# Kernel optimization log

Measured on AMD Instinct MI355X. Metric: run time of the kernel, lower is better.

The kernel has to match this reference:

```python
import jax, jax.numpy as jnp
import numpy as np

N, E, B = 100000, 1600000, 1024
F, H, C = 9, 4, 32
CH, L = 30, 20

def _leaky(x, slope):
    return jnp.where(x >= 0, x, slope * x)

def _add_self_loops(edge_index, n):
    ar = jnp.arange(n, dtype=edge_index.dtype)
    return jnp.concatenate([edge_index, jnp.stack([ar, ar])], axis=1)

def _gat_conv(x, edge_index, W, att_src, att_dst, bias):
    # PyG GATConv, concat heads, eval mode (no attn dropout), self loops
    n = x.shape[0]
    ei = _add_self_loops(edge_index, n)
    src, dst = ei[0], ei[1]
    h = (x @ W).reshape(n, H, C)                      # [N,H,C]
    a_s = jnp.sum(h * att_src, axis=-1)               # [N,H]
    a_d = jnp.sum(h * att_dst, axis=-1)               # [N,H]
    e = _leaky(a_s[src] + a_d[dst], 0.2)              # [Etot,H]
    m = jax.ops.segment_max(e, dst, num_segments=n)
    ex = jnp.exp(e - m[dst])
    s = jax.ops.segment_sum(ex, dst, num_segments=n)
    alpha = ex / (s[dst] + 1e-16)                     # softmax per dst node/head
    msg = h[src] * alpha[:, :, None]                  # [Etot,H,C]
    out = jax.ops.segment_sum(msg, dst, num_segments=n)
    return out.reshape(n, H * C) + bias

def _gcn_conv(x, edge_index, W, bias):
    # PyG GCNConv: self loops + symmetric normalization
    n = x.shape[0]
    ei = _add_self_loops(edge_index, n)
    src, dst = ei[0], ei[1]
    deg = jax.ops.segment_sum(jnp.ones(ei.shape[1], x.dtype), dst, num_segments=n)
    dinv = jnp.where(deg > 0, jax.lax.rsqrt(deg), 0.0)
    norm = dinv[src] * dinv[dst]                      # [Etot]
    h = x @ W
    out = jax.ops.segment_sum(h[src] * norm[:, None], dst, num_segments=n)
    return out + bias

def _global_mean_pool(x, batch, b):
    s = jax.ops.segment_sum(x, batch, num_segments=b)
    cnt = jax.ops.segment_sum(jnp.ones(x.shape[0], x.dtype), batch, num_segments=b)
    return s / jnp.maximum(cnt, 1.0)[:, None]

def _conv1d(x, w, b):
    # x: [B,Cin,L], w: [Cout,Cin,K], VALID conv
    y = jax.lax.conv_general_dilated(x, w, (1,), 'VALID',
                                     dimension_numbers=('NCH', 'OIH', 'NCH'))
    return y + b[None, :, None]

def _bn_eval(x, g, be, m, v):
    return (x - m[None, :, None]) * jax.lax.rsqrt(v[None, :, None] + 1e-5) * g[None, :, None] + be[None, :, None]

def _forward(x, seq_data, W_gat, att_src, att_dst, b_gat, W2, b2, W3, b3,
             conv1_w, conv1_b, conv2_w, conv2_b,
             bn1_g, bn1_b, bn1_m, bn1_v, bn2_g, bn2_b, bn2_m, bn2_v,
             fc1_W, fc1_b, fus_W, fus_b, cls1_W, cls1_b, cls3_W, cls3_b,
             edge_index, batch):
    slope = 0.01  # nn.LeakyReLU default
    # graph branch
    g = _leaky(_gat_conv(x, edge_index, W_gat, att_src, att_dst, b_gat), slope)
    g = _leaky(_gcn_conv(g, edge_index, W2, b2), slope)
    g = _leaky(_gcn_conv(g, edge_index, W3, b3), slope)
    g = _global_mean_pool(g, batch, B)                # [B,128]
    # sequence branch (eval mode: dropout = identity, BN uses running stats)
    s = _conv1d(seq_data, conv1_w, conv1_b)           # [B,64,18]
    s = _leaky(_bn_eval(s, bn1_g, bn1_b, bn1_m, bn1_v), slope)
    s = _conv1d(s, conv2_w, conv2_b)                  # [B,64,16]
    s = _leaky(_bn_eval(s, bn2_g, bn2_b, bn2_m, bn2_v), slope)
    s = s.reshape(s.shape[0], -1) @ fc1_W + fc1_b     # [B,64]
    # fusion + classifier
    comb = jnp.concatenate([g, s], axis=1)            # [B,192]
    comb = _leaky(comb @ fus_W + fus_b, slope)
    comb = _leaky(comb @ cls1_W + cls1_b, slope)
    return comb @ cls3_W + cls3_b                     # [B,1]

def setup_inputs():
    key = jax.random.key(0)
    ks = jax.random.split(key, 20)
    rn = lambda k, s, sc=0.1: jax.random.normal(k, s, dtype=jnp.float32) * sc
    return {
        'x': rn(ks[0], (N, F), 1.0),
        'edge_index': jax.random.randint(ks[1], (2, E), 0, N, dtype=jnp.int32),
        'batch': jnp.sort(jax.random.randint(ks[2], (N,), 0, B, dtype=jnp.int32)),
        'seq_data': rn(ks[3], (B, CH, L), 1.0),
        'W_gat': rn(ks[4], (F, H * C)), 'att_src': rn(ks[5], (H, C)),
        'att_dst': rn(ks[6], (H, C)), 'b_gat': jnp.zeros(H * C, jnp.float32),
        'W2': rn(ks[7], (H * C, 64)), 'b2': jnp.zeros(64, jnp.float32),
        'W3': rn(ks[8], (64, 128)), 'b3': jnp.zeros(128, jnp.float32),
        'conv1_w': rn(ks[9], (64, CH, 3)), 'conv1_b': jnp.zeros(64, jnp.float32),
        'conv2_w': rn(ks[10], (64, 64, 3)), 'conv2_b': jnp.zeros(64, jnp.float32),
        'bn1_g': jnp.ones(64, jnp.float32), 'bn1_b': jnp.zeros(64, jnp.float32),
        'bn1_m': jnp.zeros(64, jnp.float32), 'bn1_v': jnp.ones(64, jnp.float32),
        'bn2_g': jnp.ones(64, jnp.float32), 'bn2_b': jnp.zeros(64, jnp.float32),
        'bn2_m': jnp.zeros(64, jnp.float32), 'bn2_v': jnp.ones(64, jnp.float32),
        'fc1_W': rn(ks[11], (16 * 64, 64)), 'fc1_b': jnp.zeros(64, jnp.float32),
        'fus_W': rn(ks[12], (192, 128)), 'fus_b': jnp.zeros(128, jnp.float32),
        'cls1_W': rn(ks[13], (128, 64)), 'cls1_b': jnp.zeros(64, jnp.float32),
        'cls3_W': rn(ks[14], (64, 1)), 'cls3_b': jnp.zeros(1, jnp.float32),
    }

def reference(x, edge_index, batch, seq_data, W_gat, att_src, att_dst, b_gat,
              W2, b2, W3, b3, conv1_w, conv1_b, conv2_w, conv2_b,
              bn1_g, bn1_b, bn1_m, bn1_v, bn2_g, bn2_b, bn2_m, bn2_v,
              fc1_W, fc1_b, fus_W, fus_b, cls1_W, cls1_b, cls3_W, cls3_b):
    return _forward(x, seq_data, W_gat, att_src, att_dst, b_gat, W2, b2, W3, b3,
                    conv1_w, conv1_b, conv2_w, conv2_b,
                    bn1_g, bn1_b, bn1_m, bn1_v, bn2_g, bn2_b, bn2_m, bn2_v,
                    fc1_W, fc1_b, fus_W, fus_b, cls1_W, cls1_b, cls3_W, cls3_b,
                    edge_index, batch)
```

## Files before the change

kernel.cpp:

```cpp
#include <hip/hip_runtime.h>

#define NND 100000
#define NED 1600000
#define NB  1024
#define FEAT 9
#define HC 128
#define NBUCK ((NND + 511) / 512)
#define BCAP 12288u
#define BINCHUNK 4096
#define BIN_NBLK ((NED + BINCHUNK - 1) / BINCHUNK)

typedef unsigned short u16;

__device__ __forceinline__ void atomAdd(float* p, float v) {
    __hip_atomic_fetch_add(p, v, __ATOMIC_RELAXED, __HIP_MEMORY_SCOPE_AGENT);
}
__device__ __forceinline__ unsigned atomAddU(unsigned* p, unsigned v) {
    return __hip_atomic_fetch_add(p, v, __ATOMIC_RELAXED, __HIP_MEMORY_SCOPE_AGENT);
}
__device__ __forceinline__ float leaky(float v, float s) { return v >= 0.f ? v : s * v; }
__device__ __forceinline__ float bf2f(u16 u) {
    union { unsigned i; float f; } x; x.i = ((unsigned)u) << 16; return x.f;
}
__device__ __forceinline__ u16 f2bf(float f) {
    union { float f; unsigned i; } x; x.f = f;
    return (u16)((x.i + 0x7fffu + ((x.i >> 16) & 1u)) >> 16);
}
__device__ __forceinline__ float bflo(unsigned u) {
    union { unsigned i; float f; } x; x.i = u << 16; return x.f;
}
__device__ __forceinline__ float bfhi(unsigned u) {
    union { unsigned i; float f; } x; x.i = u & 0xffff0000u; return x.f;
}

__global__ void k_matt(const float* __restrict__ Wg, const float* __restrict__ attS,
                       const float* __restrict__ attD, float* __restrict__ M) {
    int t = threadIdx.x;
    if (t >= 72) return;
    int d = t >= 36 ? 1 : 0;
    int q = t - 36 * d;
    int f = q >> 2, h = q & 3;
    const float* av = d ? attD : attS;
    float s = 0.f;
#pragma unroll
    for (int c = 0; c < 32; ++c) s += Wg[f * HC + h * 32 + c] * av[h * 32 + c];
    M[d * 36 + q] = s;
}

__global__ void k_w2t(const float* __restrict__ W2, u16* __restrict__ w2t,
                      unsigned* __restrict__ bktCur) {
    int i = blockIdx.x * 256 + threadIdx.x;
    int n = i >> 7, k = i & 127;
    w2t[i] = f2bf(W2[k * 64 + n]);
    if (i < NBUCK) bktCur[i] = (unsigned)i * BCAP;
}

__global__ void k_att(const float* __restrict__ x, const float* __restrict__ M,
                      u16* __restrict__ rec, float* __restrict__ a_d) {
    __shared__ float Ms[36], Md[36];
    int t = threadIdx.x;
    if (t < 36) Ms[t] = M[t];
    else if (t < 72) Md[t - 36] = M[t];
    __syncthreads();
    int n = blockIdx.x * 256 + t;
    if (n >= NND) return;
    float xv[FEAT];
#pragma unroll
    for (int f = 0; f < FEAT; ++f) xv[f] = x[n * FEAT + f];
    float s0 = 0, s1 = 0, s2 = 0, s3 = 0, d0 = 0, d1 = 0, d2 = 0, d3 = 0;
#pragma unroll
    for (int f = 0; f < FEAT; ++f) {
        float xf = xv[f];
        s0 += xf * Ms[f * 4 + 0]; s1 += xf * Ms[f * 4 + 1];
        s2 += xf * Ms[f * 4 + 2]; s3 += xf * Ms[f * 4 + 3];
        d0 += xf * Md[f * 4 + 0]; d1 += xf * Md[f * 4 + 1];
        d2 += xf * Md[f * 4 + 2]; d3 += xf * Md[f * 4 + 3];
    }
    u16 v[16];
#pragma unroll
    for (int f = 0; f < FEAT; ++f) v[f] = f2bf(xv[f]);
    v[9] = f2bf(s0); v[10] = f2bf(s1); v[11] = f2bf(s2); v[12] = f2bf(s3);
    v[13] = 0; v[14] = 0; v[15] = 0;
    unsigned pk[8];
#pragma unroll
    for (int i = 0; i < 8; ++i) pk[i] = (unsigned)v[2 * i] | ((unsigned)v[2 * i + 1] << 16);
    uint4* rp = (uint4*)(rec + (size_t)n * 16);
    rp[0] = make_uint4(pk[0], pk[1], pk[2], pk[3]);
    rp[1] = make_uint4(pk[4], pk[5], pk[6], pk[7]);
    ((float4*)a_d)[n] = make_float4(d0, d1, d2, d3);
}

__global__ __launch_bounds__(256) void k_bin(const int* __restrict__ ei,
                                             unsigned* __restrict__ bktCursor,
                                             unsigned* __restrict__ staging) {
    __shared__ unsigned hist[NBUCK];
    __shared__ unsigned gbase[NBUCK];
    int t = threadIdx.x;
    if (t < NBUCK) hist[t] = 0;
    __syncthreads();
    int base = blockIdx.x * BINCHUNK;
    int lim = NED - base;
    int srcv[16], dstv[16];
#pragma unroll
    for (int k = 0; k < 16; ++k) {
        int i = t + k * 256;
        if (i < lim) {
            srcv[k] = ei[base + i];
            dstv[k] = ei[NED + base + i];
            atomicAdd(&hist[dstv[k] >> 9], 1u);
        } else dstv[k] = -1;
    }
    __syncthreads();
    if (t < NBUCK) {
        unsigned c = hist[t];
        gbase[t] = c ? atomAddU(&bktCursor[t], c) : 0u;
    }
    __syncthreads();
    if (t < NBUCK) hist[t] = 0;
    __syncthreads();
#pragma unroll
    for (int k = 0; k < 16; ++k) {
        if (dstv[k] >= 0) {
            int bk = dstv[k] >> 9;
            unsigned off = atomicAdd(&hist[bk], 1u);
            staging[gbase[bk] + off] = ((unsigned)(dstv[k] & 511) << 17) | (unsigned)srcv[k];
        }
    }
}

__global__ __launch_bounds__(512) void k_place(const unsigned* __restrict__ bktCur,
                                               const unsigned* __restrict__ staging,
                                               unsigned* __restrict__ csr,
                                               unsigned* __restrict__ rowptr,
                                               u16* __restrict__ degA,
                                               float* __restrict__ dinv) {
    __shared__ unsigned lh[512];
    __shared__ unsigned ls[512];
    int b = blockIdx.x, t = threadIdx.x;
    unsigned lo = (unsigned)b * BCAP;
    unsigned n = bktCur[b] - lo;
    lh[t] = 0;
    __syncthreads();
    for (unsigned i = t; i < n; i += 512) atomicAdd(&lh[staging[lo + i] >> 17], 1u);
    __syncthreads();
    unsigned v = lh[t];
    ls[t] = v;
    __syncthreads();
    for (int off = 1; off < 512; off <<= 1) {
        unsigned u = (t >= off) ? ls[t - off] : 0u;
        __syncthreads();
        ls[t] += u;
        __syncthreads();
    }
    unsigned excl = ls[t] - v;
    int node = b * 512 + t;
    if (node < NND) {
        rowptr[node] = lo + excl;
        degA[node] = (u16)v;
        dinv[node] = rsqrtf((float)v + 1.f);
    }
    __syncthreads();
    lh[t] = excl;
    __syncthreads();
    for (unsigned i = t; i < n; i += 512) {
        unsigned p = staging[lo + i];
        unsigned pos = atomicAdd(&lh[p >> 17], 1u);
        csr[lo + pos] = p & 0x1FFFFu;
    }
}

__global__ __launch_bounds__(256) void k_gat_g(const unsigned* __restrict__ rowptr,
                                               const u16* __restrict__ degA,
                                               const unsigned* __restrict__ csr,
                                               const u16* __restrict__ rec,
                                               const float* __restrict__ a_d,
                                               float* __restrict__ z) {
    int t = threadIdx.x;
    if (t >= 252) return;
    int g = t / 36, r = t - g * 36;
    int n = blockIdx.x * 7 + g;
    if (n >= NND) return;
    int h = r / 9, f = r - h * 9;
    unsigned e0 = rowptr[n], e1 = e0 + degA[n];
    float adh = a_d[n * 4 + h];
    size_t q = (size_t)n * 16;
    float ws = __expf(leaky(bf2f(rec[q + 9 + h]) + adh, 0.2f));
    float acc = ws * bf2f(rec[q + f]);
    float den = ws;
    unsigned e = e0;
    for (; e + 4 <= e1; e += 4) {
        size_t s0 = (size_t)csr[e] * 16, s1 = (size_t)csr[e + 1] * 16;
        size_t s2 = (size_t)csr[e + 2] * 16, s3 = (size_t)csr[e + 3] * 16;
        float a0 = bf2f(rec[s0 + 9 + h]), x0 = bf2f(rec[s0 + f]);
        float a1 = bf2f(rec[s1 + 9 + h]), x1 = bf2f(rec[s1 + f]);
        float a2 = bf2f(rec[s2 + 9 + h]), x2 = bf2f(rec[s2 + f]);
        float a3 = bf2f(rec[s3 + 9 + h]), x3 = bf2f(rec[s3 + f]);
        float w0 = __expf(leaky(a0 + adh, 0.2f));
        float w1 = __expf(leaky(a1 + adh, 0.2f));
        float w2 = __expf(leaky(a2 + adh, 0.2f));
        float w3 = __expf(leaky(a3 + adh, 0.2f));
        acc += w0 * x0 + w1 * x1 + w2 * x2 + w3 * x3;
        den += w0 + w1 + w2 + w3;
    }
    for (; e < e1; ++e) {
        size_t s = (size_t)csr[e] * 16;
        float w = __expf(leaky(bf2f(rec[s + 9 + h]) + adh, 0.2f));
        acc += w * bf2f(rec[s + f]);
        den += w;
    }
    z[n * 36 + r] = acc / (den + 1e-16f);
}

typedef __attribute__((ext_vector_type(8))) short bfrag;
typedef __attribute__((ext_vector_type(4))) float ffrag;
__global__ __launch_bounds__(256) void k_fused_h2(const float* __restrict__ z,
                                                  const float* __restrict__ Wg,
                                                  const float* __restrict__ bg,
                                                  const u16* __restrict__ w2t,
                                                  const float* __restrict__ dinv,
                                                  u16* __restrict__ h2) {
    __shared__ float zL[64 * 36];
    __shared__ float Wf[FEAT * HC];
    __shared__ float bgs[HC];
    __shared__ u16 g1L[64 * 136];
    int t = threadIdx.x;
    int n0 = blockIdx.x * 64;
    for (int i = t; i < 64 * 36; i += 256) {
        int row = i / 36;
        zL[i] = (n0 + row < NND) ? z[(size_t)(n0 + row) * 36 + (i - row * 36)] : 0.f;
    }
    for (int i = t; i < FEAT * HC; i += 256) Wf[i] = Wg[i];
    if (t < HC) bgs[t] = bg[t];
    __syncthreads();
    for (int e = t; e < 64 * 128; e += 256) {
        int row = e >> 7, col = e & 127;
        int h = col >> 5;
        float acc = bgs[col];
        const float* zr = zL + row * 36 + h * 9;
#pragma unroll
        for (int f = 0; f < 9; ++f) acc += zr[f] * Wf[f * 128 + col];
        g1L[row * 136 + col] = f2bf(leaky(acc, 0.01f));
    }
    __syncthreads();
    int l = t & 63, wv = t >> 6;
    int mr = l & 15, quad = l >> 4;
    union U { uint4 u; bfrag v; };
    bfrag a[4];
#pragma unroll
    for (int ks = 0; ks < 4; ++ks) {
        U uu; uu.u = *(const uint4*)(g1L + (wv * 16 + mr) * 136 + ks * 32 + quad * 8);
        a[ks] = uu.v;
    }
    ffrag acc[4];
#pragma unroll
    for (int ct = 0; ct < 4; ++ct) acc[ct] = (ffrag){0.f, 0.f, 0.f, 0.f};
#pragma unroll
    for (int ct = 0; ct < 4; ++ct) {
#pragma unroll
        for (int ks = 0; ks < 4; ++ks) {
            U ub; ub.u = *(const uint4*)(w2t + (ct * 16 + mr) * 128 + ks * 32 + quad * 8);
            acc[ct] = __builtin_amdgcn_mfma_f32_16x16x32_bf16(a[ks], ub.v, acc[ct], 0, 0, 0);
        }
    }
    int rbase = n0 + wv * 16 + quad * 4;
    if (rbase < NND) {
        float4 d4 = *(const float4*)(dinv + rbase);
        const float dv[4] = {d4.x, d4.y, d4.z, d4.w};
#pragma unroll
        for (int ct = 0; ct < 4; ++ct)
#pragma unroll
            for (int r = 0; r < 4; ++r)
                h2[(size_t)(rbase + r) * 64 + ct * 16 + mr] = f2bf(dv[r] * acc[ct][r]);
    }
}

template <int OUTMODE>
__global__ void k_gcn_g(const unsigned* __restrict__ rowptr, const u16* __restrict__ degA,
                        const unsigned* __restrict__ csr,
                        const float* __restrict__ dinv, const u16* __restrict__ hin,
                        const float* __restrict__ bias, u16* __restrict__ hout) {
    int n = blockIdx.x * 4 + (threadIdx.x >> 6);
    int l = threadIdx.x & 63;
    int half = l >> 5;
    int c = l & 31;
    unsigned e0 = rowptr[n];
    unsigned e1 = e0 + degA[n];
    const unsigned* hinU = (const unsigned*)hin;
    float acc0 = 0.f, acc1 = 0.f;
    if (half == 0) {
        unsigned u = hinU[(size_t)n * 32 + c];
        acc0 = bflo(u); acc1 = bfhi(u);
    }
    unsigned e = e0;
    for (; e + 8 <= e1; e += 8) {
        unsigned i0 = csr[e + half];
        unsigned i1 = csr[e + 2 + half];
        unsigned i2 = csr[e + 4 + half];
        unsigned i3 = csr[e + 6 + half];
        unsigned u0 = hinU[(size_t)i0 * 32 + c];
        unsigned u1 = hinU[(size_t)i1 * 32 + c];
        unsigned u2 = hinU[(size_t)i2 * 32 + c];
        unsigned u3 = hinU[(size_t)i3 * 32 + c];
        acc0 += bflo(u0) + bflo(u1) + bflo(u2) + bflo(u3);
        acc1 += bfhi(u0) + bfhi(u1) + bfhi(u2) + bfhi(u3);
    }
    for (; e + 2 <= e1; e += 2) {
        unsigned u = hinU[(size_t)csr[e + half] * 32 + c];
        acc0 += bflo(u); acc1 += bfhi(u);
    }
    if (e < e1 && half == 0) {
        unsigned u = hinU[(size_t)csr[e] * 32 + c];
        acc0 += bflo(u); acc1 += bfhi(u);
    }
    acc0 += __shfl_xor(acc0, 32, 64);
    acc1 += __shfl_xor(acc1, 32, 64);
    if (half == 0) {
        float dn = dinv[n];
        float o0 = dn * acc0, o1 = dn * acc1;
        if (OUTMODE == 1) {
            o0 = leaky(o0 + bias[2 * c], 0.01f) * dn;
            o1 = leaky(o1 + bias[2 * c + 1], 0.01f) * dn;
        }
        unsigned pk = (unsigned)f2bf(o0) | ((unsigned)f2bf(o1) << 16);
        ((unsigned*)hout)[(size_t)n * 32 + c] = pk;
    }
}

__global__ __launch_bounds__(128) void k_gcn2_pool(const u16* __restrict__ agg3,
                                                   const float* __restrict__ W3,
                                                   const float* __restrict__ b3,
                                                   const int* __restrict__ batch,
                                                   float* __restrict__ pooled,
                                                   float* __restrict__ cnt) {
    __shared__ float rows[64][64];
    __shared__ int bts[64];
    int t = threadIdx.x;
    int n0 = blockIdx.x * 64;
    int nn = NND - n0; if (nn > 64) nn = 64;
    const unsigned* srcp = (const unsigned*)(agg3 + (size_t)n0 * 64);
    for (int i = t; i < nn * 32; i += 128) {
        unsigned u = srcp[i];
        ((float*)rows)[2 * i]     = bf2f((u16)(u & 0xffffu));
        ((float*)rows)[2 * i + 1] = bf2f((u16)(u >> 16));
    }
    if (t < nn) bts[t] = batch[n0 + t];
    float w[64];
#pragma unroll
    for (int k = 0; k < 64; ++k) w[k] = W3[k * 128 + t];
    float bc = b3[t];
    __syncthreads();
    float pacc = 0.f, pcnt = 0.f;
    int curb = -1;
    for (int j = 0; j < nn; ++j) {
        const float4* r4 = (const float4*)rows[j];
        float acc = bc;
#pragma unroll
        for (int kk = 0; kk < 16; ++kk) {
            float4 r = r4[kk];
            acc += r.x * w[4 * kk] + r.y * w[4 * kk + 1] + r.z * w[4 * kk + 2] + r.w * w[4 * kk + 3];
        }
        float g = leaky(acc, 0.01f);
        int b = bts[j];
        if (b != curb) {
            if (curb >= 0) {
                atomAdd(&pooled[curb * 128 + t], pacc);
                if (t == 0) atomAdd(&cnt[curb], pcnt);
            }
            curb = b; pacc = 0.f; pcnt = 0.f;
        }
        pacc += g; pcnt += 1.f;
    }
    if (curb >= 0) {
        atomAdd(&pooled[curb * 128 + t], pacc);
        if (t == 0) atomAdd(&cnt[curb], pcnt);
    }
}

__global__ void k_seq(const float* __restrict__ seq, const float* __restrict__ w1, const float* __restrict__ c1b,
                      const float* __restrict__ w2, const float* __restrict__ c2b,
                      const float* __restrict__ g1n, const float* __restrict__ b1n,
                      const float* __restrict__ m1n, const float* __restrict__ v1n,
                      const float* __restrict__ g2n, const float* __restrict__ b2n,
                      const float* __restrict__ m2n, const float* __restrict__ v2n,
                      const float* __restrict__ fcW, const float* __restrict__ fcb,
                      float* __restrict__ sfc) {
    __shared__ float xs[30 * 20];
    __shared__ float y1[64 * 18];
    __shared__ float y2[64 * 16];
    __shared__ float red[4][64];
    int t = threadIdx.x;
    int b = blockIdx.x;
    for (int idx = t; idx < 600; idx += 256) xs[idx] = seq[b * 600 + idx];
    __syncthreads();
    for (int idx = t; idx < 64 * 18; idx += 256) {
        int o = idx / 18, l = idx - o * 18;
        float acc = c1b[o];
        for (int i = 0; i < 30; ++i)
#pragma unroll
            for (int k = 0; k < 3; ++k)
                acc += xs[i * 20 + l + k] * w1[o * 90 + i * 3 + k];
        float bn = (acc - m1n[o]) * rsqrtf(v1n[o] + 1e-5f) * g1n[o] + b1n[o];
        y1[idx] = leaky(bn, 0.01f);
    }
    __syncthreads();
    for (int idx = t; idx < 64 * 16; idx += 256) {
        int o = idx >> 4, l = idx & 15;
        float acc = c2b[o];
        for (int i = 0; i < 64; ++i)
#pragma unroll
            for (int k = 0; k < 3; ++k)
                acc += y1[i * 18 + l + k] * w2[o * 192 + i * 3 + k];
        float bn = (acc - m2n[o]) * rsqrtf(v2n[o] + 1e-5f) * g2n[o] + b2n[o];
        y2[idx] = leaky(bn, 0.01f);
    }
    __syncthreads();
    {
        int o = t & 63, part = t >> 6;
        float acc = 0.f;
        for (int j = part * 256; j < part * 256 + 256; ++j)
            acc += y2[j] * fcW[j * 64 + o];
        red[part][o] = acc;
    }
    __syncthreads();
    if (t < 64) sfc[b * 64 + t] = red[0][t] + red[1][t] + red[2][t] + red[3][t] + fcb[t];
}

__global__ void k_final(const float* __restrict__ pooled, const float* __restrict__ cnt,
                        const float* __restrict__ sfc,
                        const float* __restrict__ fusW, const float* __restrict__ fusb,
                        const float* __restrict__ c1W, const float* __restrict__ c1b,
                        const float* __restrict__ c3W, const float* __restrict__ c3b,
                        float* __restrict__ out) {
    __shared__ float comb[192];
    __shared__ float t1[128];
    int t = threadIdx.x;
    int b = blockIdx.x;
    float invc = 1.f / fmaxf(cnt[b], 1.f);
    comb[t] = pooled[b * 128 + t] * invc;
    if (t < 64) comb[128 + t] = sfc[b * 64 + t];
    __syncthreads();
    float acc = fusb[t];
    for (int k = 0; k < 192; ++k) acc += comb[k] * fusW[k * 128 + t];
    t1[t] = leaky(acc, 0.01f);
    __syncthreads();
    if (t < 64) {
        float a2 = c1b[t];
        for (int k = 0; k < 128; ++k) a2 += t1[k] * c1W[k * 64 + t];
        a2 = leaky(a2, 0.01f);
        float p = a2 * c3W[t];
#pragma unroll
        for (int off = 32; off; off >>= 1) p += __shfl_xor(p, off, 64);
        if (t == 0) out[b] = p + c3b[0];
    }
}

extern "C" void kernel_launch(void* const* d_in, const int* in_sizes, int n_in,
                              void* d_out, int out_size, void* d_ws, size_t ws_size,
                              hipStream_t stream) {
    const float* x     = (const float*)d_in[0];
    const int*   ei    = (const int*)d_in[1];
    const int*   batch = (const int*)d_in[2];
    const float* seq   = (const float*)d_in[3];
    const float* Wg    = (const float*)d_in[4];
    const float* attS  = (const float*)d_in[5];
    const float* attD  = (const float*)d_in[6];
    const float* bg    = (const float*)d_in[7];
    const float* W2    = (const float*)d_in[8];
    const float* b2    = (const float*)d_in[9];
    const float* W3    = (const float*)d_in[10];
    const float* b3    = (const float*)d_in[11];
    const float* c1w   = (const float*)d_in[12];
    const float* c1bb  = (const float*)d_in[13];
    const float* c2w   = (const float*)d_in[14];
    const float* c2bb  = (const float*)d_in[15];
    const float* bn1g  = (const float*)d_in[16];
    const float* bn1b  = (const float*)d_in[17];
    const float* bn1m  = (const float*)d_in[18];
    const float* bn1v  = (const float*)d_in[19];
    const float* bn2g  = (const float*)d_in[20];
    const float* bn2b  = (const float*)d_in[21];
    const float* bn2m  = (const float*)d_in[22];
    const float* bn2v  = (const float*)d_in[23];
    const float* fcW   = (const float*)d_in[24];
    const float* fcb   = (const float*)d_in[25];
    const float* fusW  = (const float*)d_in[26];
    const float* fusb  = (const float*)d_in[27];
    const float* cls1W = (const float*)d_in[28];
    const float* cls1b = (const float*)d_in[29];
    const float* cls3W = (const float*)d_in[30];
    const float* cls3b = (const float*)d_in[31];

    char* wsb = (char*)d_ws;
    const size_t N = NND;
    float*    M      = (float*)wsb;
    float*    a_d    = M + 80;
    u16*      rec    = (u16*)(a_d + N * 4);
    float*    dinv   = (float*)(rec + N * 16);
    float*    pooled = dinv + N;
    float*    cnt    = pooled + (size_t)NB * 128;
    unsigned* bktCur = (unsigned*)(cnt + NB);
    unsigned* rowptr = bktCur + 256;
    u16*      degA   = (u16*)(rowptr + N);
    u16*      w2t    = degA + N + 8;
    unsigned* staging= (unsigned*)(w2t + 8192);
    unsigned* csr    = staging + (size_t)NBUCK * BCAP;
    float*    z      = (float*)(csr + (size_t)NBUCK * BCAP);
    u16*      h2b    = (u16*)(z + N * 36 + 64);
    u16*      g2b    = h2b + N * 64;
    u16*      agg3b  = g2b + N * 64;
    float*    sfc    = (float*)(agg3b + N * 64);

    size_t zero_bytes = ((size_t)NB * 128 + NB) * 4;
    hipMemsetAsync(pooled, 0, zero_bytes, stream);

    k_matt<<<1, 128, 0, stream>>>(Wg, attS, attD, M);
    k_w2t<<<32, 256, 0, stream>>>(W2, w2t, bktCur);
    k_att<<<(NND + 255) / 256, 256, 0, stream>>>(x, M, rec, a_d);
    k_bin<<<BIN_NBLK, 256, 0, stream>>>(ei, bktCur, staging);
    k_place<<<NBUCK, 512, 0, stream>>>(bktCur, staging, csr, rowptr, degA, dinv);
    k_gat_g<<<(NND + 6) / 7, 256, 0, stream>>>(rowptr, degA, csr, rec, a_d, z);
    k_fused_h2<<<(NND + 63) / 64, 256, 0, stream>>>(z, Wg, bg, w2t, dinv, h2b);
    k_gcn_g<1><<<NND / 4, 256, 0, stream>>>(rowptr, degA, csr, dinv, h2b, b2, g2b);
    k_gcn_g<0><<<NND / 4, 256, 0, stream>>>(rowptr, degA, csr, dinv, g2b, b2, agg3b);
    k_gcn2_pool<<<(NND + 63) / 64, 128, 0, stream>>>(agg3b, W3, b3, batch, pooled, cnt);
    k_seq<<<NB, 256, 0, stream>>>(seq, c1w, c1bb, c2w, c2bb, bn1g, bn1b, bn1m, bn1v,
                                  bn2g, bn2b, bn2m, bn2v, fcW, fcb, sfc);
    k_final<<<NB, 128, 0, stream>>>(pooled, cnt, sfc, fusW, fusb, cls1W, cls1b,
                                    cls3W, cls3b, (float*)d_out);
}
```

Measured before the change: 472.3 us.

## Parallelize GAT gather over edges per wavefront and widen GCN gather loads

The GAT aggregation kernel now assigns one wavefront per node, with lanes split across 16 edges and 4 heads. Each lane loads a whole 32-byte source record (features plus attention logits, now moved into the upper record slots) and reduces across lanes with shuffles. Before, there was one thread per (head, feature), each doing scalar bf16 loads. The GCN gather also moves from 2 edge groups with 4-byte loads to 4 edge groups with 8-byte loads. The goal is better memory-level parallelism and fewer, wider loads, at the cost of shuffle reductions and idle lanes on low-degree nodes.

New measurement: 455.5 us. -3.5%, faster.

```diff
diff --git a/kernel.cpp b/kernel.cpp
--- a/kernel.cpp
+++ b/kernel.cpp
@@ -79,8 +79,8 @@
     u16 v[16];
 #pragma unroll
     for (int f = 0; f < FEAT; ++f) v[f] = f2bf(xv[f]);
-    v[9] = f2bf(s0); v[10] = f2bf(s1); v[11] = f2bf(s2); v[12] = f2bf(s3);
-    v[13] = 0; v[14] = 0; v[15] = 0;
+    v[9] = 0; v[10] = 0; v[11] = 0;
+    v[12] = f2bf(s0); v[13] = f2bf(s1); v[14] = f2bf(s2); v[15] = f2bf(s3);
     unsigned pk[8];
 #pragma unroll
     for (int i = 0; i < 8; ++i) pk[i] = (unsigned)v[2 * i] | ((unsigned)v[2 * i + 1] << 16);
@@ -175,40 +175,54 @@
                                                const u16* __restrict__ rec,
                                                const float* __restrict__ a_d,
                                                float* __restrict__ z) {
-    int t = threadIdx.x;
-    if (t >= 252) return;
-    int g = t / 36, r = t - g * 36;
-    int n = blockIdx.x * 7 + g;
-    if (n >= NND) return;
-    int h = r / 9, f = r - h * 9;
-    unsigned e0 = rowptr[n], e1 = e0 + degA[n];
+    int n = blockIdx.x * 4 + (threadIdx.x >> 6);
+    int l = threadIdx.x & 63;
+    int e = l >> 2;
+    int h = l & 3;
+    unsigned e0 = rowptr[n];
+    int m = (int)degA[n] + 1;
     float adh = a_d[n * 4 + h];
-    size_t q = (size_t)n * 16;
-    float ws = __expf(leaky(bf2f(rec[q + 9 + h]) + adh, 0.2f));
-    float acc = ws * bf2f(rec[q + f]);
-    float den = ws;
-    unsigned e = e0;
-    for (; e + 4 <= e1; e += 4) {
-        size_t s0 = (size_t)csr[e] * 16, s1 = (size_t)csr[e + 1] * 16;
-        size_t s2 = (size_t)csr[e + 2] * 16, s3 = (size_t)csr[e + 3] * 16;
-        float a0 = bf2f(rec[s0 + 9 + h]), x0 = bf2f(rec[s0 + f]);
-        float a1 = bf2f(rec[s1 + 9 + h]), x1 = bf2f(rec[s1 + f]);
-        float a2 = bf2f(rec[s2 + 9 + h]), x2 = bf2f(rec[s2 + f]);
-        float a3 = bf2f(rec[s3 + 9 + h]), x3 = bf2f(rec[s3 + f]);
-        float w0 = __expf(leaky(a0 + adh, 0.2f));
-        float w1 = __expf(leaky(a1 + adh, 0.2f));
-        float w2 = __expf(leaky(a2 + adh, 0.2f));
-        float w3 = __expf(leaky(a3 + adh, 0.2f));
-        acc += w0 * x0 + w1 * x1 + w2 * x2 + w3 * x3;
-        den += w0 + w1 + w2 + w3;
-    }
-    for (; e < e1; ++e) {
-        size_t s = (size_t)csr[e] * 16;
-        float w = __expf(leaky(bf2f(rec[s + 9 + h]) + adh, 0.2f));
-        acc += w * bf2f(rec[s + f]);
+    float acc0 = 0, acc1 = 0, acc2 = 0, acc3 = 0, acc4 = 0, acc5 = 0, acc6 = 0, acc7 = 0, acc8 = 0;
+    float den = 0.f;
+    const uint4* recp = (const uint4*)rec;
+    for (int c = 0; c < m; c += 16) {
+        int idx = c + e;
+        bool act = idx < m;
+        int src = n;
+        if (act && idx > 0) src = (int)csr[e0 + idx - 1];
+        uint4 lo = recp[(size_t)src * 2];
+        uint4 hi = recp[(size_t)src * 2 + 1];
+        unsigned pair = (h & 2) ? hi.w : hi.z;
+        float asf = (h & 1) ? bfhi(pair) : bflo(pair);
+        float w = __expf(leaky(asf + adh, 0.2f));
+        if (!act) w = 0.f;
         den += w;
-    }
-    z[n * 36 + r] = acc / (den + 1e-16f);
+        acc0 += w * bflo(lo.x); acc1 += w * bfhi(lo.x);
+        acc2 += w * bflo(lo.y); acc3 += w * bfhi(lo.y);
+        acc4 += w * bflo(lo.z); acc5 += w * bfhi(lo.z);
+        acc6 += w * bflo(lo.w); acc7 += w * bfhi(lo.w);
+        acc8 += w * bflo(hi.x);
+    }
+#pragma unroll
+    for (int mask = 4; mask <= 32; mask <<= 1) {
+        den  += __shfl_xor(den,  mask, 64);
+        acc0 += __shfl_xor(acc0, mask, 64);
+        acc1 += __shfl_xor(acc1, mask, 64);
+        acc2 += __shfl_xor(acc2, mask, 64);
+        acc3 += __shfl_xor(acc3, mask, 64);
+        acc4 += __shfl_xor(acc4, mask, 64);
+        acc5 += __shfl_xor(acc5, mask, 64);
+        acc6 += __shfl_xor(acc6, mask, 64);
+        acc7 += __shfl_xor(acc7, mask, 64);
+        acc8 += __shfl_xor(acc8, mask, 64);
+    }
+    if (l < 4) {
+        float inv = 1.f / (den + 1e-16f);
+        float* zp = z + (size_t)n * 36 + h * 9;
+        zp[0] = acc0 * inv; zp[1] = acc1 * inv; zp[2] = acc2 * inv;
+        zp[3] = acc3 * inv; zp[4] = acc4 * inv; zp[5] = acc5 * inv;
+        zp[6] = acc6 * inv; zp[7] = acc7 * inv; zp[8] = acc8 * inv;
+    }
 }
 
 typedef __attribute__((ext_vector_type(8))) short bfrag;
@@ -281,48 +295,55 @@
                         const float* __restrict__ bias, u16* __restrict__ hout) {
     int n = blockIdx.x * 4 + (threadIdx.x >> 6);
     int l = threadIdx.x & 63;
-    int half = l >> 5;
-    int c = l & 31;
+    int grp = l >> 4;
+    int c = l & 15;
     unsigned e0 = rowptr[n];
     unsigned e1 = e0 + degA[n];
-    const unsigned* hinU = (const unsigned*)hin;
-    float acc0 = 0.f, acc1 = 0.f;
-    if (half == 0) {
-        unsigned u = hinU[(size_t)n * 32 + c];
-        acc0 = bflo(u); acc1 = bfhi(u);
+    const uint2* hinU = (const uint2*)hin;
+    float a0 = 0, a1 = 0, a2 = 0, a3 = 0;
+    if (grp == 0) {
+        uint2 u = hinU[(size_t)n * 16 + c];
+        a0 = bflo(u.x); a1 = bfhi(u.x); a2 = bflo(u.y); a3 = bfhi(u.y);
     }
     unsigned e = e0;
     for (; e + 8 <= e1; e += 8) {
-        unsigned i0 = csr[e + half];
-        unsigned i1 = csr[e + 2 + half];
-        unsigned i2 = csr[e + 4 + half];
-        unsigned i3 = csr[e + 6 + half];
-        unsigned u0 = hinU[(size_t)i0 * 32 + c];
-        unsigned u1 = hinU[(size_t)i1 * 32 + c];
-        unsigned u2 = hinU[(size_t)i2 * 32 + c];
-        unsigned u3 = hinU[(size_t)i3 * 32 + c];
-        acc0 += bflo(u0) + bflo(u1) + bflo(u2) + bflo(u3);
-        acc1 += bfhi(u0) + bfhi(u1) + bfhi(u2) + bfhi(u3);
-    }
-    for (; e + 2 <= e1; e += 2) {
-        unsigned u = hinU[(size_t)csr[e + half] * 32 + c];
-        acc0 += bflo(u); acc1 += bfhi(u);
-    }
-    if (e < e1 && half == 0) {
-        unsigned u = hinU[(size_t)csr[e] * 32 + c];
-        acc0 += bflo(u); acc1 += bfhi(u);
-    }
-    acc0 += __shfl_xor(acc0, 32, 64);
-    acc1 += __shfl_xor(acc1, 32, 64);
-    if (half == 0) {
+        unsigned s0 = csr[e + grp];
+        unsigned s1 = csr[e + 4 + grp];
+        uint2 u0 = hinU[(size_t)s0 * 16 + c];
+        uint2 u1 = hinU[(size_t)s1 * 16 + c];
+        a0 += bflo(u0.x) + bflo(u1.x); a1 += bfhi(u0.x) + bfhi(u1.x);
+        a2 += bflo(u0.y) + bflo(u1.y); a3 += bfhi(u0.y) + bfhi(u1.y);
+    }
+    for (; e + 4 <= e1; e += 4) {
+        unsigned s = csr[e + grp];
+        uint2 u = hinU[(size_t)s * 16 + c];
+        a0 += bflo(u.x); a1 += bfhi(u.x); a2 += bflo(u.y); a3 += bfhi(u.y);
+    }
+    if (grp < (int)(e1 - e)) {
+        unsigned s = csr[e + grp];
+        uint2 u = hinU[(size_t)s * 16 + c];
+        a0 += bflo(u.x); a1 += bfhi(u.x); a2 += bflo(u.y); a3 += bfhi(u.y);
+    }
+#pragma unroll
+    for (int mask = 16; mask <= 32; mask <<= 1) {
+        a0 += __shfl_xor(a0, mask, 64);
+        a1 += __shfl_xor(a1, mask, 64);
+        a2 += __shfl_xor(a2, mask, 64);
+        a3 += __shfl_xor(a3, mask, 64);
+    }
+    if (grp == 0) {
         float dn = dinv[n];
-        float o0 = dn * acc0, o1 = dn * acc1;
+        float o0 = dn * a0, o1 = dn * a1, o2 = dn * a2, o3 = dn * a3;
         if (OUTMODE == 1) {
-            o0 = leaky(o0 + bias[2 * c], 0.01f) * dn;
-            o1 = leaky(o1 + bias[2 * c + 1], 0.01f) * dn;
+            o0 = leaky(o0 + bias[4 * c],     0.01f) * dn;
+            o1 = leaky(o1 + bias[4 * c + 1], 0.01f) * dn;
+            o2 = leaky(o2 + bias[4 * c + 2], 0.01f) * dn;
+            o3 = leaky(o3 + bias[4 * c + 3], 0.01f) * dn;
         }
-        unsigned pk = (unsigned)f2bf(o0) | ((unsigned)f2bf(o1) << 16);
-        ((unsigned*)hout)[(size_t)n * 32 + c] = pk;
+        uint2 pk;
+        pk.x = (unsigned)f2bf(o0) | ((unsigned)f2bf(o1) << 16);
+        pk.y = (unsigned)f2bf(o2) | ((unsigned)f2bf(o3) << 16);
+        ((uint2*)hout)[(size_t)n * 16 + c] = pk;
     }
 }
 
@@ -518,7 +539,7 @@
     k_att<<<(NND + 255) / 256, 256, 0, stream>>>(x, M, rec, a_d);
     k_bin<<<BIN_NBLK, 256, 0, stream>>>(ei, bktCur, staging);
     k_place<<<NBUCK, 512, 0, stream>>>(bktCur, staging, csr, rowptr, degA, dinv);
-    k_gat_g<<<(NND + 6) / 7, 256, 0, stream>>>(rowptr, degA, csr, rec, a_d, z);
+    k_gat_g<<<NND / 4, 256, 0, stream>>>(rowptr, degA, csr, rec, a_d, z);
     k_fused_h2<<<(NND + 63) / 64, 256, 0, stream>>>(z, Wg, bg, w2t, dinv, h2b);
     k_gcn_g<1><<<NND / 4, 256, 0, stream>>>(rowptr, degA, csr, dinv, h2b, b2, g2b);
     k_gcn_g<0><<<NND / 4, 256, 0, stream>>>(rowptr, degA, csr, dinv, g2b, b2, agg3b);
```
